# Kernel optimization log

Hardware: AMD Instinct MI355X
Metric: run time of the kernel (lower is better)

The kernel has to match this reference:

```python
import jax, jax.numpy as jnp
import numpy as np

K = 16
NS = [2048, 512, 128]

def _knn(q, r, k):
    # q: [B,M,3] query centers, r: [B,N,3] reference points -> (idx [B,M,k], sqdist [B,M,k])
    d2 = (jnp.sum(q * q, -1)[:, :, None] + jnp.sum(r * r, -1)[:, None, :]
          - 2.0 * jnp.einsum('bmd,bnd->bmn', q, r))
    neg, idx = jax.lax.top_k(-d2, k)
    return idx, jnp.maximum(-neg, 0.0)

def _gather(feat, idx):
    # feat [B,N,C], idx [B,M,k] -> [B,M,k,C]
    return jax.vmap(lambda f, i: f[i])(feat, idx)

def _down(x, pos, n, W1, b1, W2, b2):
    # PointNet++-style TransitionDown: sample n centers, kNN group, rel-pos concat, shared MLP, max-pool
    centers = pos[:, :n]
    idx, _ = _knn(centers, pos, K)
    rel = _gather(pos, idx) - centers[:, :, None, :]           # [B,n,K,3]
    feat = jnp.concatenate([rel, _gather(x, idx)], -1)          # [B,n,K,C+3]
    h = jax.nn.relu(feat @ W1 + b1) @ W2 + b2                   # last_act=False
    return jnp.max(h, axis=2), centers

def _up(xc, pc, prv_feat, prv_pos, W, b):
    # TransitionUp: 3-NN inverse-distance interpolation + skip concat + pointwise conv1d
    idx, d2 = _knn(prv_pos, pc, 3)
    w = 1.0 / (d2 + 1e-8)
    w = w / jnp.sum(w, -1, keepdims=True)
    interp = jnp.sum(_gather(xc, idx) * w[..., None], axis=2)   # [B,Nprv,Cc]
    cat = jnp.concatenate([interp, prv_feat], -1)
    return jax.nn.relu(cat @ W + b)

def setup_inputs() -> dict:
    key = jax.random.key(0)
    ks = jax.random.split(key, 16)
    p = lambda k, s: jax.random.normal(k, s, jnp.float32) * 0.02
    B, N = 4, 8192
    return {
        'x': jax.random.normal(ks[0], (B, N, 3), jnp.float32),
        'pos': jax.random.uniform(ks[1], (B, N, 3), jnp.float32),
        'd0_W1': p(ks[2], (6, 128)),   'd0_b1': jnp.zeros((128,), jnp.float32),
        'd0_W2': p(ks[3], (128, 128)), 'd0_b2': jnp.zeros((128,), jnp.float32),
        'd1_W1': p(ks[4], (131, 256)), 'd1_b1': jnp.zeros((256,), jnp.float32),
        'd1_W2': p(ks[5], (256, 256)), 'd1_b2': jnp.zeros((256,), jnp.float32),
        'd2_W1': p(ks[6], (259, 512)), 'd2_b1': jnp.zeros((512,), jnp.float32),
        'd2_W2': p(ks[7], (512, 512)), 'd2_b2': jnp.zeros((512,), jnp.float32),
        'u0_W': p(ks[8], (768, 256)),  'u0_b': jnp.zeros((256,), jnp.float32),
        'u1_W': p(ks[9], (384, 128)),  'u1_b': jnp.zeros((128,), jnp.float32),
        'u2_W': p(ks[10], (134, 128)), 'u2_b': jnp.zeros((128,), jnp.float32),
        'f_W1': p(ks[11], (128, 128)), 'f_b1': jnp.zeros((128,), jnp.float32),
        'f_W2': p(ks[12], (128, 128)), 'f_b2': jnp.zeros((128,), jnp.float32),
    }

def reference(x, pos, d0_W1, d0_b1, d0_W2, d0_b2, d1_W1, d1_b1, d1_W2, d1_b2,
              d2_W1, d2_b1, d2_W2, d2_b2, u0_W, u0_b, u1_W, u1_b, u2_W, u2_b,
              f_W1, f_b1, f_W2, f_b2):
    pos0, x0 = pos, x
    # encoder (transition-down) with cached (pos, x) per scale
    x1, pos1 = _down(x0, pos0, NS[0], d0_W1, d0_b1, d0_W2, d0_b2)
    x2, pos2 = _down(x1, pos1, NS[1], d1_W1, d1_b1, d1_W2, d1_b2)
    x3, pos3 = _down(x2, pos2, NS[2], d2_W1, d2_b1, d2_W2, d2_b2)
    # decoder (transition-up) consuming the cache in reverse; last level concats raw pos to skip feat
    up = _up(x3, pos3, x2, pos2, u0_W, u0_b)
    up = _up(up, pos2, x1, pos1, u1_W, u1_b)
    prv0 = jnp.concatenate([x0, pos0], -1)
    up = _up(up, pos1, prv0, pos0, u2_W, u2_b)
    # feat_map_layer_out: two pointwise conv1d layers, last_act=False
    out = jax.nn.relu(up @ f_W1 + f_b1) @ f_W2 + f_b2
    return (out, pos0)
```

## Files before the change

kernel.cpp:

```cpp
#include <hip/hip_runtime.h>

#define NFULL 8192
#define BATCH 4

typedef unsigned long long u64;
typedef unsigned int u32;
typedef __attribute__((ext_vector_type(8))) short bf8_t;
typedef __attribute__((ext_vector_type(4))) float f4_t;

__device__ __forceinline__ u32 fbias(float f) {
  u32 u = __float_as_uint(f);
  return (u & 0x80000000u) ? ~u : (u | 0x80000000u);
}
__device__ __forceinline__ float funbias(u32 b) {
  u32 u = (b & 0x80000000u) ? (b & 0x7fffffffu) : ~b;
  return __uint_as_float(u);
}
__device__ __forceinline__ short f2bf(float f) {
  u32 u = __float_as_uint(f);
  u32 r = u + 0x7FFFu + ((u >> 16) & 1u);
  return (short)(r >> 16);
}

__device__ __forceinline__ void group_insert_g32(u32 m32, u64 ck, int slot16,
                                                 u64& val, u64& tau) {
  if (m32) {
    while (m32) {
      int src = __ffs(m32) - 1;
      m32 &= m32 - 1;
      u64 c = __shfl((unsigned long long)ck, src, 32);
      u64 prev = __shfl_up((unsigned long long)val, 1, 16);
      if (slot16 == 0) prev = 0ull;
      val = (val <= c) ? val : ((prev <= c) ? c : prev);
    }
    tau = __shfl((unsigned long long)val, 15, 16);
  }
}

__device__ __forceinline__ void first_round_sort32(u64 ck, int gl,
                                                   u64& val, u64& tau) {
  u64 v = ck;
#pragma unroll
  for (int size = 2; size <= 32; size <<= 1) {
#pragma unroll
    for (int stride = size >> 1; stride > 0; stride >>= 1) {
      u64 other = __shfl_xor((unsigned long long)v, stride, 32);
      bool ddd = ((gl & size) == 0);
      bool takeMin = (((gl & stride) == 0) == ddd);
      u64 mn = (v <= other) ? v : other;
      u64 mx = (v <= other) ? other : v;
      v = takeMin ? mn : mx;
    }
  }
  val = __shfl((unsigned long long)v, gl & 15, 32);
  tau = __shfl((unsigned long long)val, 15, 16);
}

__device__ __forceinline__ void scan_range_g32(const float4* __restrict__ sb,
    int s, int e, float qx, float qy, float qz, float qq,
    int g32, int gl, int slot16, u64& val, u64& tau) {
  for (int t0 = s; t0 < e; t0 += 32) {
    int j = t0 + gl;
    u64 ck = ~0ull;
    if (j < e) {
      float4 P = sb[j];
      float rr = P.x * P.x + P.y * P.y + P.z * P.z;
      float d2 = qq + rr - 2.0f * (qx * P.x + qy * P.y + qz * P.z);
      ck = ((u64)fbias(d2) << 32) | (u32)__float_as_uint(P.w);
    }
    u64 full = __ballot(ck < tau);
    u32 m32 = (u32)(full >> (g32 * 32));
    group_insert_g32(m32, ck, slot16, val, tau);
  }
}

template<int GR, int R, int NREF>
__device__ __forceinline__ void knn_tail16_g32(
    const float4* __restrict__ sb, const int* __restrict__ cs,
    float qx, float qy, float qz, float qq,
    int ix, int iy, int iz, int x0, int x1, int y0, int y1, int z0, int z1,
    int g32, int gl, int slot16, u64& val, u64& tau) {
  const float h = 1.0f / GR;
  float m = 1e30f;
  if (x0 > 0)      m = fminf(m, qx - x0 * h);
  if (x1 < GR - 1) m = fminf(m, (x1 + 1) * h - qx);
  if (y0 > 0)      m = fminf(m, qy - y0 * h);
  if (y1 < GR - 1) m = fminf(m, (y1 + 1) * h - qy);
  if (z0 > 0)      m = fminf(m, qz - z0 * h);
  if (z1 < GR - 1) m = fminf(m, (z1 + 1) * h - qz);
  float bound = m * m;
  float kth_d2 = funbias((u32)(tau >> 32));
  if (!(kth_d2 < bound)) {
    int X0 = max(ix - (R + 1), 0), X1 = min(ix + (R + 1), GR - 1);
    int Y0 = max(iy - (R + 1), 0), Y1 = min(iy + (R + 1), GR - 1);
    int Z0 = max(iz - (R + 1), 0), Z1 = min(iz + (R + 1), GR - 1);
    int NY2 = Y1 - Y0 + 1;
    int nrow2 = (Z1 - Z0 + 1) * NY2;
    for (int rr2 = 0; rr2 < nrow2; ++rr2) {
      int zz = Z0 + rr2 / NY2, yy = Y0 + rr2 % NY2;
      int c0 = (zz * GR + yy) * GR;
      bool mid = (zz >= z0 && zz <= z1 && yy >= y0 && yy <= y1);
      int s1 = cs[c0 + X0];
      int e1 = mid ? cs[c0 + x0] : cs[c0 + X1 + 1];
      scan_range_g32(sb, s1, e1, qx, qy, qz, qq, g32, gl, slot16, val, tau);
      if (mid) {
        int s2 = cs[c0 + x1 + 1];
        int e2 = cs[c0 + X1 + 1];
        scan_range_g32(sb, s2, e2, qx, qy, qz, qq, g32, gl, slot16, val, tau);
      }
    }
    x0 = X0; x1 = X1; y0 = Y0; y1 = Y1; z0 = Z0; z1 = Z1;
    m = 1e30f;
    if (x0 > 0)      m = fminf(m, qx - x0 * h);
    if (x1 < GR - 1) m = fminf(m, (x1 + 1) * h - qx);
    if (y0 > 0)      m = fminf(m, qy - y0 * h);
    if (y1 < GR - 1) m = fminf(m, (y1 + 1) * h - qy);
    if (z0 > 0)      m = fminf(m, qz - z0 * h);
    if (z1 < GR - 1) m = fminf(m, (z1 + 1) * h - qz);
    bound = m * m;
    kth_d2 = funbias((u32)(tau >> 32));
    if (!(kth_d2 < bound)) {
      for (int t0 = 0; t0 < NREF; t0 += 32) {
        int j = t0 + gl;
        u64 ck = ~0ull;
        if (j < NREF) {
          float4 P = sb[j];
          int cx = min(max((int)(P.x * GR), 0), GR - 1);
          int cy = min(max((int)(P.y * GR), 0), GR - 1);
          int cz = min(max((int)(P.z * GR), 0), GR - 1);
          bool inbox = (cx >= x0 && cx <= x1 && cy >= y0 && cy <= y1 &&
                        cz >= z0 && cz <= z1);
          if (!inbox) {
            float rr = P.x * P.x + P.y * P.y + P.z * P.z;
            float d2 = qq + rr - 2.0f * (qx * P.x + qy * P.y + qz * P.z);
            ck = ((u64)fbias(d2) << 32) | (u32)__float_as_uint(P.w);
          }
        }
        u64 full = __ballot(ck < tau);
        u32 m32 = (u32)(full >> (g32 * 32));
        group_insert_g32(m32, ck, slot16, val, tau);
      }
    }
  }
}

template<int GR, int R, int NREF>
__device__ void knn_grid16_g32_dev(int vbx, int b,
    const float* __restrict__ pos, const float4* __restrict__ sorted,
    const int* __restrict__ cellStart, int csStride, int Mq,
    int* __restrict__ oidx) {
  int wv = threadIdx.x >> 6, lane = threadIdx.x & 63;
  int g32 = lane >> 5, gl = lane & 31;
  int q = vbx * 8 + wv * 2 + g32;
  const float* pb = pos + (size_t)b * NFULL * 3;
  const float4* sb = sorted + (size_t)b * NREF;
  const int* cs = cellStart + b * csStride;
  float qx = pb[q * 3 + 0], qy = pb[q * 3 + 1], qz = pb[q * 3 + 2];
  float qq = qx * qx + qy * qy + qz * qz;
  int ix = min(max((int)(qx * GR), 0), GR - 1);
  int iy = min(max((int)(qy * GR), 0), GR - 1);
  int iz = min(max((int)(qz * GR), 0), GR - 1);
  int x0 = max(ix - R, 0), x1 = min(ix + R, GR - 1);
  int y0 = max(iy - R, 0), y1 = min(iy + R, GR - 1);
  int z0 = max(iz - R, 0), z1 = min(iz + R, GR - 1);

  int ny = y1 - y0 + 1;
  int nrow = (z1 - z0 + 1) * ny;
  int s_i = 0, len_i = 0;
  if (gl < nrow) {
    int zz = z0 + gl / ny, yy = y0 + gl % ny;
    int c0 = (zz * GR + yy) * GR + x0;
    s_i = cs[c0];
    len_i = cs[c0 + (x1 - x0) + 1] - s_i;
  }
  int p_i = len_i;
#pragma unroll
  for (int st = 1; st < 32; st <<= 1) {
    int o = __shfl_up(p_i, st, 32);
    if (gl >= st) p_i += o;
  }
  int T = __shfl(p_i, 31, 32);
  p_i -= len_i;
  int d_i = s_i - p_i;
  if (gl >= nrow) p_i = 0x7fffffff;

  int slot16 = lane & 15;
  u64 val, tau;

  {
    int v = gl;
    int r = 0;
#pragma unroll
    for (int st = 16; st >= 1; st >>= 1) {
      int pc = __shfl(p_i, r + st, 32);
      if (v >= pc) r += st;
    }
    int addr = v + __shfl(d_i, r, 32);
    u64 ck = ~0ull;
    if (v < T) {
      float4 P = sb[addr];
      float rr = P.x * P.x + P.y * P.y + P.z * P.z;
      float d2 = qq + rr - 2.0f * (qx * P.x + qy * P.y + qz * P.z);
      ck = ((u64)fbias(d2) << 32) | (u32)__float_as_uint(P.w);
    }
    first_round_sort32(ck, gl, val, tau);
  }

  for (int v0 = 32; v0 < T; v0 += 32) {
    int v = v0 + gl;
    int r = 0;
#pragma unroll
    for (int st = 16; st >= 1; st >>= 1) {
      int pc = __shfl(p_i, r + st, 32);
      if (v >= pc) r += st;
    }
    int addr = v + __shfl(d_i, r, 32);
    u64 ck = ~0ull;
    if (v < T) {
      float4 P = sb[addr];
      float rr = P.x * P.x + P.y * P.y + P.z * P.z;
      float d2 = qq + rr - 2.0f * (qx * P.x + qy * P.y + qz * P.z);
      ck = ((u64)fbias(d2) << 32) | (u32)__float_as_uint(P.w);
    }
    u64 full = __ballot(ck < tau);
    u32 m32 = (u32)(full >> (g32 * 32));
    group_insert_g32(m32, ck, slot16, val, tau);
  }

  knn_tail16_g32<GR, R, NREF>(sb, cs, qx, qy, qz, qq,
      ix, iy, iz, x0, x1, y0, y1, z0, z1, g32, gl, slot16, val, tau);

  if (gl < 16) {
    size_t base = ((size_t)b * Mq + q) * 16;
    oidx[base + gl] = (int)(u32)val;
  }
}

__device__ void knn_brute16_g32_dev(int vbx, int b,
    const float* __restrict__ pos, int Nref, int Mq, int* __restrict__ oidx) {
  int wv = threadIdx.x >> 6, lane = threadIdx.x & 63;
  int g32 = lane >> 5, gl = lane & 31;
  int q = vbx * 8 + wv * 2 + g32;
  const float* pb = pos + (size_t)b * NFULL * 3;
  float qx = pb[q * 3 + 0], qy = pb[q * 3 + 1], qz = pb[q * 3 + 2];
  float qq = qx * qx + qy * qy + qz * qz;

  int slot16 = lane & 15;
  u64 val, tau;

  {
    int j = gl;
    float rx = pb[j * 3 + 0];
    float ry = pb[j * 3 + 1];
    float rz = pb[j * 3 + 2];
    float rr = rx * rx + ry * ry + rz * rz;
    float d2 = qq + rr - 2.0f * (qx * rx + qy * ry + qz * rz);
    u64 ck = ((u64)fbias(d2) << 32) | (u32)j;
    first_round_sort32(ck, gl, val, tau);
  }

  for (int t0 = 32; t0 < Nref; t0 += 32) {
    int j = t0 + gl;
    float rx = pb[j * 3 + 0];
    float ry = pb[j * 3 + 1];
    float rz = pb[j * 3 + 2];
    float rr = rx * rx + ry * ry + rz * rz;
    float d2 = qq + rr - 2.0f * (qx * rx + qy * ry + qz * rz);
    u64 ck = ((u64)fbias(d2) << 32) | (u32)j;
    u64 full = __ballot(ck < tau);
    u32 m32 = (u32)(full >> (g32 * 32));
    group_insert_g32(m32, ck, slot16, val, tau);
  }

  if (gl < 16) {
    size_t base = ((size_t)b * Mq + q) * 16;
    oidx[base + gl] = (int)(u32)val;
  }
}

__device__ __forceinline__ void lane_insert3(u64 ck, u64& v0, u64& v1, u64& v2) {
  u64 a = (v0 <= ck) ? v0 : ck;
  u64 bb = (v0 <= ck) ? ck : v0;
  v0 = a;
  u64 c = (v1 <= bb) ? v1 : bb;
  u64 d = (v1 <= bb) ? bb : v1;
  v1 = c;
  v2 = (v2 <= d) ? v2 : d;
}

__device__ __forceinline__ void merge3(u64 v0, u64 v1, u64 v2,
                                       u64& o0, u64& o1, u64& o2) {
  u64 h = v0;
  int hc = 0;
  u64 outs[3];
#pragma unroll
  for (int k = 0; k < 3; ++k) {
    u64 m = h;
#pragma unroll
    for (int st = 1; st < 16; st <<= 1) {
      u64 o = __shfl_xor((unsigned long long)m, st, 16);
      m = (m <= o) ? m : o;
    }
    outs[k] = m;
    if (h == m) { ++hc; h = (hc == 1) ? v1 : ((hc == 2) ? v2 : ~0ull); }
  }
  o0 = outs[0]; o1 = outs[1]; o2 = outs[2];
}

__device__ __forceinline__ void scan_range3(const float4* __restrict__ sb,
    int s, int e, float qx, float qy, float qz, float qq,
    int gl, u64& v0, u64& v1, u64& v2) {
  for (int t0 = s; t0 < e; t0 += 16) {
    int j = t0 + gl;
    if (j < e) {
      float4 P = sb[j];
      float rr = P.x * P.x + P.y * P.y + P.z * P.z;
      float d2 = qq + rr - 2.0f * (qx * P.x + qy * P.y + qz * P.z);
      u64 ck = ((u64)fbias(d2) << 32) | (u32)__float_as_uint(P.w);
      lane_insert3(ck, v0, v1, v2);
    }
  }
}

template<int GR, int R, int NREF>
__device__ __forceinline__ void knn_tail3(
    const float4* __restrict__ sb, const int* __restrict__ cs,
    float qx, float qy, float qz, float qq,
    int ix, int iy, int iz, int x0, int x1, int y0, int y1, int z0, int z1,
    int gl, u64& v0, u64& v1, u64& v2, u64& o0, u64& o1, u64& o2) {
  const float h = 1.0f / GR;
  float m = 1e30f;
  if (x0 > 0)      m = fminf(m, qx - x0 * h);
  if (x1 < GR - 1) m = fminf(m, (x1 + 1) * h - qx);
  if (y0 > 0)      m = fminf(m, qy - y0 * h);
  if (y1 < GR - 1) m = fminf(m, (y1 + 1) * h - qy);
  if (z0 > 0)      m = fminf(m, qz - z0 * h);
  if (z1 < GR - 1) m = fminf(m, (z1 + 1) * h - qz);
  float bound = m * m;
  merge3(v0, v1, v2, o0, o1, o2);
  float kth_d2 = funbias((u32)(o2 >> 32));
  if (!(kth_d2 < bound)) {
    int X0 = max(ix - (R + 1), 0), X1 = min(ix + (R + 1), GR - 1);
    int Y0 = max(iy - (R + 1), 0), Y1 = min(iy + (R + 1), GR - 1);
    int Z0 = max(iz - (R + 1), 0), Z1 = min(iz + (R + 1), GR - 1);
    int NY2 = Y1 - Y0 + 1;
    int nrow2 = (Z1 - Z0 + 1) * NY2;
    for (int rr2 = 0; rr2 < nrow2; ++rr2) {
      int zz = Z0 + rr2 / NY2, yy = Y0 + rr2 % NY2;
      int c0 = (zz * GR + yy) * GR;
      bool mid = (zz >= z0 && zz <= z1 && yy >= y0 && yy <= y1);
      int s1 = cs[c0 + X0];
      int e1 = mid ? cs[c0 + x0] : cs[c0 + X1 + 1];
      scan_range3(sb, s1, e1, qx, qy, qz, qq, gl, v0, v1, v2);
      if (mid) {
        int s2 = cs[c0 + x1 + 1];
        int e2 = cs[c0 + X1 + 1];
        scan_range3(sb, s2, e2, qx, qy, qz, qq, gl, v0, v1, v2);
      }
    }
    x0 = X0; x1 = X1; y0 = Y0; y1 = Y1; z0 = Z0; z1 = Z1;
    m = 1e30f;
    if (x0 > 0)      m = fminf(m, qx - x0 * h);
    if (x1 < GR - 1) m = fminf(m, (x1 + 1) * h - qx);
    if (y0 > 0)      m = fminf(m, qy - y0 * h);
    if (y1 < GR - 1) m = fminf(m, (y1 + 1) * h - qy);
    if (z0 > 0)      m = fminf(m, qz - z0 * h);
    if (z1 < GR - 1) m = fminf(m, (z1 + 1) * h - qz);
    bound = m * m;
    merge3(v0, v1, v2, o0, o1, o2);
    kth_d2 = funbias((u32)(o2 >> 32));
    if (!(kth_d2 < bound)) {
      for (int t0 = 0; t0 < NREF; t0 += 16) {
        int j = t0 + gl;
        if (j < NREF) {
          float4 P = sb[j];
          int cx = min(max((int)(P.x * GR), 0), GR - 1);
          int cy = min(max((int)(P.y * GR), 0), GR - 1);
          int cz = min(max((int)(P.z * GR), 0), GR - 1);
          bool inbox = (cx >= x0 && cx <= x1 && cy >= y0 && cy <= y1 &&
                        cz >= z0 && cz <= z1);
          if (!inbox) {
            float rr = P.x * P.x + P.y * P.y + P.z * P.z;
            float d2 = qq + rr - 2.0f * (qx * P.x + qy * P.y + qz * P.z);
            u64 ck = ((u64)fbias(d2) << 32) | (u32)__float_as_uint(P.w);
            lane_insert3(ck, v0, v1, v2);
          }
        }
// ... 174 lines not shown
  float qx = pb[q * 3 + 0], qy = pb[q * 3 + 1], qz = pb[q * 3 + 2];
  float qq = qx * qx + qy * qy + qz * qz;

  u64 v0 = ~0ull, v1 = ~0ull, v2 = ~0ull;
  for (int j = gl; j < Nref; j += 16) {
    float rx = pb[j * 3 + 0];
    float ry = pb[j * 3 + 1];
    float rz = pb[j * 3 + 2];
    float rr = rx * rx + ry * ry + rz * rz;
    float d2 = qq + rr - 2.0f * (qx * rx + qy * ry + qz * rz);
    u64 ck = ((u64)fbias(d2) << 32) | (u32)j;
    lane_insert3(ck, v0, v1, v2);
  }
  u64 o0, o1, o2;
  merge3(v0, v1, v2, o0, o1, o2);

  if (gl < 3) {
    u64 val = (gl == 0) ? o0 : ((gl == 1) ? o1 : o2);
    size_t base = ((size_t)b * Mq + q) * 3;
    oidx[base + gl] = (int)(u32)val;
    od2[base + gl] = fmaxf(funbias((u32)(val >> 32)), 0.0f);
  }
}

__device__ __forceinline__ void pack_tile_rt(const float* __restrict__ W,
                                             short* __restrict__ outp,
                                             int KDIM, int N, int tile, int lane) {
  int NT = N >> 4;
  int kt = tile / NT, nt = tile - kt * NT;
  int n = nt * 16 + (lane & 15);
  int k0 = kt * 32 + (lane >> 4) * 8;
  bf8_t v;
#pragma unroll
  for (int j = 0; j < 8; ++j) {
    int k = k0 + j;
    v[j] = (k < KDIM) ? f2bf(W[(size_t)k * N + n]) : (short)0;
  }
  *(bf8_t*)(outp + ((size_t)tile * 64 + lane) * 8) = v;
}

__device__ void pack_dispatch(int blk, int lane,
    const float* d0W1, short* d0W1p, const float* d0W2, short* d0W2p,
    const float* d1W1, short* d1W1p, const float* d1W2, short* d1W2p,
    const float* d2W1, short* d2W1p, const float* d2W2, short* d2W2p,
    const float* u2W, short* u2Wp, const float* fW1, short* fW1p,
    const float* fW2, short* fW2p,
    const float* u0W, short* u0Wp, const float* u1W, short* u1Wp,
    const float* pos, float* posOut) {
  if      (blk < 8)    pack_tile_rt(d0W1, d0W1p, 6, 128, blk, lane);
  else if (blk < 40)   pack_tile_rt(d0W2, d0W2p, 128, 128, blk - 8, lane);
  else if (blk < 120)  pack_tile_rt(d1W1, d1W1p, 131, 256, blk - 40, lane);
  else if (blk < 248)  pack_tile_rt(d1W2, d1W2p, 256, 256, blk - 120, lane);
  else if (blk < 536)  pack_tile_rt(d2W1, d2W1p, 259, 512, blk - 248, lane);
  else if (blk < 1048) pack_tile_rt(d2W2, d2W2p, 512, 512, blk - 536, lane);
  else if (blk < 1088) pack_tile_rt(u2W, u2Wp, 134, 128, blk - 1048, lane);
  else if (blk < 1120) pack_tile_rt(fW1, fW1p, 128, 128, blk - 1088, lane);
  else if (blk < 1152) pack_tile_rt(fW2, fW2p, 128, 128, blk - 1120, lane);
  else if (blk < 1536) pack_tile_rt(u0W, u0Wp, 768, 256, blk - 1152, lane);
  else if (blk < 1632) pack_tile_rt(u1W, u1Wp, 384, 128, blk - 1536, lane);
  else {
    int base = (blk - 1632) * 256;
#pragma unroll
    for (int j = 0; j < 4; ++j) {
      int i = base + lane + j * 64;
      posOut[i] = pos[i];
    }
  }
}

__global__ __launch_bounds__(256) void pre_kernel(
    const float* __restrict__ pos, float4* __restrict__ sortedA,
    int* __restrict__ csA, float4* __restrict__ sortedB, int* __restrict__ csB,
    float4* __restrict__ sortedC, int* __restrict__ csC,
    const float* d0W1, short* d0W1p, const float* d0W2, short* d0W2p,
    const float* d1W1, short* d1W1p, const float* d1W2, short* d1W2p,
    const float* d2W1, short* d2W1p, const float* d2W2, short* d2W2p,
    const float* u2W, short* u2Wp, const float* fW1, short* fW1p,
    const float* fW2, short* fW2p,
    const float* u0W, short* u0Wp, const float* u1W, short* u1Wp,
    float* posOut,
    int* __restrict__ idx2, int* __restrict__ idxu0, float* __restrict__ d2u0) {
  __shared__ int cnt[4096];
  __shared__ int partial[256];
  int bx = blockIdx.x, t = threadIdx.x;
  if (bx >= 580) {
    int i = bx - 580;
    knn_brute3_dev(i & 31, i >> 5, pos, 128, 512, idxu0, d2u0);
    return;
  }
  if (bx >= 516) {
    int i = bx - 516;
    knn_brute16_g32_dev(i & 15, i >> 4, pos, 512, 128, idx2);
    return;
  }
  if (bx >= 12) {
    int tt = (bx - 12) * 4 + (t >> 6);
    pack_dispatch(tt, t & 63,
        d0W1, d0W1p, d0W2, d0W2p, d1W1, d1W1p, d1W2, d1W2p,
        d2W1, d2W1p, d2W2, d2W2p, u2W, u2Wp, fW1, fW1p, fW2, fW2p,
        u0W, u0Wp, u1W, u1Wp, pos, posOut);
    return;
  }
  int which = bx >> 2, b = bx & 3;
  int NREF = (which == 0) ? 8192 : (which == 1) ? 2048 : 512;
  int GR = (which == 0) ? 16 : 8;
  int NC = GR * GR * GR;
  float4* sorted = ((which == 0) ? sortedA : (which == 1) ? sortedB : sortedC)
                   + (size_t)b * NREF;
  int* cs = ((which == 0) ? csA + b * 4097 : (which == 1) ? csB + b * 513
                                           : csC + b * 513);
  const float* pb = pos + (size_t)b * NFULL * 3;
  for (int c = t; c < NC; c += 256) cnt[c] = 0;
  __syncthreads();
  for (int p = t; p < NREF; p += 256) {
    float x = pb[p * 3 + 0], y = pb[p * 3 + 1], z = pb[p * 3 + 2];
    int cx = min(max((int)(x * GR), 0), GR - 1);
    int cy = min(max((int)(y * GR), 0), GR - 1);
    int cz = min(max((int)(z * GR), 0), GR - 1);
    atomicAdd(&cnt[(cz * GR + cy) * GR + cx], 1);
  }
  __syncthreads();
  int chunk = (NC + 255) / 256;
  int s = 0;
  for (int i = 0; i < chunk; ++i) {
    int c = t * chunk + i;
    if (c < NC) s += cnt[c];
  }
  partial[t] = s;
  __syncthreads();
  if (t == 0) {
    int run = 0;
    for (int i = 0; i < 256; ++i) { int v = partial[i]; partial[i] = run; run += v; }
  }
  __syncthreads();
  int run = partial[t];
  for (int i = 0; i < chunk; ++i) {
    int c = t * chunk + i;
    if (c < NC) { int v = cnt[c]; cnt[c] = run; run += v; }
  }
  __syncthreads();
  for (int c = t; c < NC; c += 256) cs[c] = cnt[c];
  if (t == 0) cs[NC] = NREF;
  __syncthreads();
  for (int p = t; p < NREF; p += 256) {
    float x = pb[p * 3 + 0], y = pb[p * 3 + 1], z = pb[p * 3 + 2];
    int cx = min(max((int)(x * GR), 0), GR - 1);
    int cy = min(max((int)(y * GR), 0), GR - 1);
    int cz = min(max((int)(z * GR), 0), GR - 1);
    int slot = atomicAdd(&cnt[(cz * GR + cy) * GR + cx], 1);
    sorted[slot] = make_float4(x, y, z, __uint_as_float((u32)p));
  }
}

__global__ __launch_bounds__(256) void knn16_kernel(
    const float* __restrict__ pos,
    const float4* __restrict__ sortedA, const int* __restrict__ csA,
    const float4* __restrict__ sortedB, const int* __restrict__ csB,
    int* __restrict__ idx0, int* __restrict__ idx1) {
  int bx = blockIdx.x, b = blockIdx.y;
  if (bx < 64)
    knn_grid16_g32_dev<8, 2, 2048>(bx, b, pos, sortedB, csB, 513, 512, idx1);
  else
    knn_grid16_g32_dev<16, 2, 8192>(bx - 64, b, pos, sortedA, csA, 4097, 2048, idx0);
}

template<int FEAT, int CIN, int CHID, int FPAD, int QB, int WAVES>
__device__ void down_mfma_body(int bxx, int b,
    const float* __restrict__ pos, const float* __restrict__ xin,
    const int* __restrict__ idx,
    const short* __restrict__ W1p, const float* __restrict__ b1,
    const short* __restrict__ W2p, const float* __restrict__ b2,
    float* __restrict__ out, int n, int nprev) {
  const int KT1 = FPAD / 32, NT1 = CHID / 16;
  const int KT2 = CHID / 32, NT2 = CHID / 16;
  __shared__ short sFeat[QB][16][FPAD + 8];
  __shared__ short sH1[QB][16][CHID + 8];
  __shared__ int sIdx[QB][16];
  __shared__ float sCtr[QB][3];
  int q0 = bxx * QB;
  int t = threadIdx.x;
  int lane = t & 63, wv = t >> 6;
  const float* pb = pos + (size_t)b * NFULL * 3;
  const float* xb = xin + (size_t)b * nprev * CIN;
  if (t < QB * 16)
    sIdx[t >> 4][t & 15] = idx[((size_t)b * n + q0 + (t >> 4)) * 16 + (t & 15)];
  if (t < QB * 3) sCtr[t / 3][t % 3] = pb[(q0 + t / 3) * 3 + (t % 3)];
  __syncthreads();
  for (int e = t; e < QB * 16 * FPAD; e += 64 * WAVES) {
    int k = e / FPAD, c = e - k * FPAD;
    int qq = k >> 4, kk = k & 15;
    float v = 0.f;
    if (c < 3) v = pb[sIdx[qq][kk] * 3 + c] - sCtr[qq][c];
    else if (c < FEAT) v = xb[(size_t)sIdx[qq][kk] * CIN + (c - 3)];
    sFeat[qq][kk][c] = f2bf(v);
  }
  __syncthreads();

  int col = lane & 15, quad = lane >> 4;
  const bf8_t* W1t = (const bf8_t*)W1p;
  for (int nt = 2 * wv; nt < NT1; nt += 2 * WAVES) {
    f4_t acc[QB][2];
    float bb0 = b1[nt * 16 + col], bb1 = b1[nt * 16 + 16 + col];
#pragma unroll
    for (int q = 0; q < QB; ++q) {
      acc[q][0] = {bb0, bb0, bb0, bb0};
      acc[q][1] = {bb1, bb1, bb1, bb1};
    }
#pragma unroll
    for (int kt = 0; kt < KT1; ++kt) {
      bf8_t bf0 = W1t[(kt * NT1 + nt) * 64 + lane];
      bf8_t bf1 = W1t[(kt * NT1 + nt + 1) * 64 + lane];
#pragma unroll
      for (int q = 0; q < QB; ++q) {
        bf8_t a = *(const bf8_t*)&sFeat[q][col][kt * 32 + quad * 8];
        acc[q][0] = __builtin_amdgcn_mfma_f32_16x16x32_bf16(a, bf0, acc[q][0], 0, 0, 0);
        acc[q][1] = __builtin_amdgcn_mfma_f32_16x16x32_bf16(a, bf1, acc[q][1], 0, 0, 0);
      }
    }
#pragma unroll
    for (int q = 0; q < QB; ++q)
#pragma unroll
      for (int r = 0; r < 4; ++r) {
        sH1[q][quad * 4 + r][nt * 16 + col] = f2bf(fmaxf(acc[q][0][r], 0.f));
        sH1[q][quad * 4 + r][nt * 16 + 16 + col] = f2bf(fmaxf(acc[q][1][r], 0.f));
      }
  }
  __syncthreads();

  const bf8_t* W2t = (const bf8_t*)W2p;
  for (int nt = 2 * wv; nt < NT2; nt += 2 * WAVES) {
    f4_t acc[QB][2];
    float bb0 = b2[nt * 16 + col], bb1 = b2[nt * 16 + 16 + col];
#pragma unroll
    for (int q = 0; q < QB; ++q) {
      acc[q][0] = {bb0, bb0, bb0, bb0};
      acc[q][1] = {bb1, bb1, bb1, bb1};
    }
#pragma unroll
    for (int kt = 0; kt < KT2; ++kt) {
      bf8_t bf0 = W2t[(kt * NT2 + nt) * 64 + lane];
      bf8_t bf1 = W2t[(kt * NT2 + nt + 1) * 64 + lane];
#pragma unroll
      for (int q = 0; q < QB; ++q) {
        bf8_t a = *(const bf8_t*)&sH1[q][col][kt * 32 + quad * 8];
        acc[q][0] = __builtin_amdgcn_mfma_f32_16x16x32_bf16(a, bf0, acc[q][0], 0, 0, 0);
        acc[q][1] = __builtin_amdgcn_mfma_f32_16x16x32_bf16(a, bf1, acc[q][1], 0, 0, 0);
      }
    }
#pragma unroll
    for (int q = 0; q < QB; ++q) {
      float m0 = fmaxf(fmaxf(acc[q][0][0], acc[q][0][1]), fmaxf(acc[q][0][2], acc[q][0][3]));
      float m1 = fmaxf(fmaxf(acc[q][1][0], acc[q][1][1]), fmaxf(acc[q][1][2], acc[q][1][3]));
      m0 = fmaxf(m0, __shfl_xor(m0, 16, 64));
      m0 = fmaxf(m0, __shfl_xor(m0, 32, 64));
      m1 = fmaxf(m1, __shfl_xor(m1, 16, 64));
      m1 = fmaxf(m1, __shfl_xor(m1, 32, 64));
      if (lane < 16) {
        float* ob = out + ((size_t)b * n + q0 + q) * CHID;
        ob[nt * 16 + lane] = m0;
        ob[nt * 16 + 16 + lane] = m1;
      }
    }
  }
}

template<int FEAT, int CIN, int CHID, int FPAD, int QB, int WAVES>
__global__ __launch_bounds__(64 * WAVES) void down_mfma_kernel(
    const float* __restrict__ pos, const float* __restrict__ xin,
    const int* __restrict__ idx,
    const short* __restrict__ W1p, const float* __restrict__ b1,
    const short* __restrict__ W2p, const float* __restrict__ b2,
    float* __restrict__ out, int n, int nprev) {
  down_mfma_body<FEAT, CIN, CHID, FPAD, QB, WAVES>(blockIdx.x, blockIdx.y,
      pos, xin, idx, W1p, b1, W2p, b2, out, n, nprev);
}

__global__ __launch_bounds__(256) void down0_knn3_kernel(
    const float* __restrict__ pos, const float* __restrict__ xin,
    const int* __restrict__ idx,
    const short* __restrict__ W1p, const float* __restrict__ b1,
    const short* __restrict__ W2p, const float* __restrict__ b2,
    float* __restrict__ out,
    const float4* __restrict__ sortedB, const int* __restrict__ csB,
    const float4* __restrict__ sortedC, const int* __restrict__ csC,
    int* __restrict__ idxu1, float* __restrict__ d2u1,
    int* __restrict__ idxu2, float* __restrict__ d2u2) {
  int bx = blockIdx.x, b = blockIdx.y;
  if (bx < 512)
    down_mfma_body<6, 3, 128, 32, 4, 4>(bx, b, pos, xin, idx,
        W1p, b1, W2p, b2, out, 2048, 8192);
  else if (bx < 1024)
    knn_grid_flat3_dev<8, 1, 2048>(bx - 512, b, pos, sortedB, csB, 513, 8192, idxu2, d2u2);
  else
    knn_grid_flat32_3_dev<8, 2, 512>(bx - 1024, b, pos, sortedC, csC, 513, 2048, idxu1, d2u1);
}

template<int CIN, int CPRV, int COUT, int WPB>
__global__ __launch_bounds__(64 * WPB) void up_mfma_kernel(
    const float* __restrict__ xc, int ncoarse,
    const int* __restrict__ idx3, const float* __restrict__ d23,
    const float* __restrict__ prv, const short* __restrict__ Wp,
    const float* __restrict__ bvec, float* __restrict__ out, int m) {
  const int CTOT = CIN + CPRV;
  const int KT = CTOT / 32, NT = COUT / 16;
  __shared__ short sA[16][CTOT + 8];
  __shared__ float sWt[16][3];
  __shared__ int   sIt[16][3];
  int b = blockIdx.y, q0 = blockIdx.x * 16, t = threadIdx.x;
  int lane = t & 63, wv = t >> 6;
  if (t < 16) {
    size_t base = ((size_t)b * m + q0 + t) * 3;
    float d0 = d23[base + 0], d1 = d23[base + 1], d2v = d23[base + 2];
    float w0 = 1.f / (d0 + 1e-8f), w1 = 1.f / (d1 + 1e-8f), w2 = 1.f / (d2v + 1e-8f);
    float s = w0 + w1 + w2;
    sWt[t][0] = w0 / s; sWt[t][1] = w1 / s; sWt[t][2] = w2 / s;
    sIt[t][0] = idx3[base + 0]; sIt[t][1] = idx3[base + 1]; sIt[t][2] = idx3[base + 2];
  }
  __syncthreads();
  const float* xb = xc + (size_t)b * ncoarse * CIN;
  const float* pvb = prv + ((size_t)b * m + q0) * CPRV;
  for (int e = t; e < 16 * CIN; e += 64 * WPB) {
    int p = e / CIN, c = e % CIN;
    float v = sWt[p][0] * xb[(size_t)sIt[p][0] * CIN + c]
            + sWt[p][1] * xb[(size_t)sIt[p][1] * CIN + c]
            + sWt[p][2] * xb[(size_t)sIt[p][2] * CIN + c];
    sA[p][c] = f2bf(v);
  }
  for (int e = t; e < 16 * CPRV; e += 64 * WPB) {
    int p = e / CPRV, c = e % CPRV;
    sA[p][CIN + c] = f2bf(pvb[(size_t)p * CPRV + c]);
  }
  __syncthreads();
  int col = lane & 15, quad = lane >> 4;
  const bf8_t* Wt = (const bf8_t*)Wp;
  float* ob = out + ((size_t)b * m + q0) * COUT;
  for (int nt = 2 * wv; nt < NT; nt += 2 * WPB) {
    float bb0 = bvec[nt * 16 + col], bb1 = bvec[nt * 16 + 16 + col];
    f4_t acc0 = {bb0, bb0, bb0, bb0}, acc1 = {bb1, bb1, bb1, bb1};
#pragma unroll
    for (int kt = 0; kt < KT; ++kt) {
      bf8_t a = *(const bf8_t*)&sA[col][kt * 32 + quad * 8];
      bf8_t bf0 = Wt[(kt * NT + nt) * 64 + lane];
      bf8_t bf1 = Wt[(kt * NT + nt + 1) * 64 + lane];
      acc0 = __builtin_amdgcn_mfma_f32_16x16x32_bf16(a, bf0, acc0, 0, 0, 0);
      acc1 = __builtin_amdgcn_mfma_f32_16x16x32_bf16(a, bf1, acc1, 0, 0, 0);
    }
#pragma unroll
    for (int r = 0; r < 4; ++r) {
      ob[(size_t)(quad * 4 + r) * COUT + nt * 16 + col] = fmaxf(acc0[r], 0.f);
      ob[(size_t)(quad * 4 + r) * COUT + nt * 16 + 16 + col] = fmaxf(acc1[r], 0.f);
    }
  }
}

__global__ __launch_bounds__(128) void up2f_mfma_kernel(
    const float* __restrict__ xc,
    const int* __restrict__ idx3, const float* __restrict__ d23,
    const float* __restrict__ x0, const float* __restrict__ pos0,
    const short* __restrict__ u2Wp, const float* __restrict__ u2b,
    const short* __restrict__ fW1p, const float* __restrict__ fb1,
    const short* __restrict__ fW2p, const float* __restrict__ fb2,
    float* __restrict__ out) {
  __shared__ short sA[16][168];
  __shared__ short sB[16][136];
  __shared__ float sWt[16][3];
  __shared__ int   sIt[16][3];
  int b = blockIdx.y, q0 = blockIdx.x * 16, t = threadIdx.x;
  int lane = t & 63, wv = t >> 6;
  if (t < 16) {
    size_t base = ((size_t)b * NFULL + q0 + t) * 3;
    float d0 = d23[base + 0], d1 = d23[base + 1], d2v = d23[base + 2];
    float w0 = 1.f / (d0 + 1e-8f), w1 = 1.f / (d1 + 1e-8f), w2 = 1.f / (d2v + 1e-8f);
    float s = w0 + w1 + w2;
    sWt[t][0] = w0 / s; sWt[t][1] = w1 / s; sWt[t][2] = w2 / s;
    sIt[t][0] = idx3[base + 0]; sIt[t][1] = idx3[base + 1]; sIt[t][2] = idx3[base + 2];
  }
  __syncthreads();
  const float* xb = xc + (size_t)b * 2048 * 128;
#pragma unroll
  for (int p = 0; p < 16; ++p) {
    float v = sWt[p][0] * xb[(size_t)sIt[p][0] * 128 + t]
            + sWt[p][1] * xb[(size_t)sIt[p][1] * 128 + t]
            + sWt[p][2] * xb[(size_t)sIt[p][2] * 128 + t];
    sA[p][t] = f2bf(v);
  }
  for (int e = t; e < 16 * 32; e += 128) {
    int p = e / 32, c = 128 + (e % 32);
    float v = 0.f;
    if (c < 131) v = x0[((size_t)b * NFULL + q0 + p) * 3 + (c - 128)];
    else if (c < 134) v = pos0[((size_t)b * NFULL + q0 + p) * 3 + (c - 131)];
    sA[p][c] = f2bf(v);
  }
  __syncthreads();
  int col = lane & 15, quad = lane >> 4;

  bf8_t a1[5];
#pragma unroll
  for (int kt = 0; kt < 5; ++kt)
    a1[kt] = *(const bf8_t*)&sA[col][kt * 32 + quad * 8];
  const bf8_t* W1t = (const bf8_t*)u2Wp;
  for (int nt = 2 * wv; nt < 8; nt += 4) {
    float bb0 = u2b[nt * 16 + col], bb1 = u2b[nt * 16 + 16 + col];
    f4_t acc0 = {bb0, bb0, bb0, bb0}, acc1 = {bb1, bb1, bb1, bb1};
#pragma unroll
    for (int kt = 0; kt < 5; ++kt) {
      bf8_t bf0 = W1t[(kt * 8 + nt) * 64 + lane];
      bf8_t bf1 = W1t[(kt * 8 + nt + 1) * 64 + lane];
      acc0 = __builtin_amdgcn_mfma_f32_16x16x32_bf16(a1[kt], bf0, acc0, 0, 0, 0);
      acc1 = __builtin_amdgcn_mfma_f32_16x16x32_bf16(a1[kt], bf1, acc1, 0, 0, 0);
    }
#pragma unroll
    for (int r = 0; r < 4; ++r) {
      sB[quad * 4 + r][nt * 16 + col] = f2bf(fmaxf(acc0[r], 0.f));
      sB[quad * 4 + r][nt * 16 + 16 + col] = f2bf(fmaxf(acc1[r], 0.f));
    }
  }
  __syncthreads();

  bf8_t a2[4];
#pragma unroll
  for (int kt = 0; kt < 4; ++kt)
    a2[kt] = *(const bf8_t*)&sB[col][kt * 32 + quad * 8];
  const bf8_t* W2t = (const bf8_t*)fW1p;
  for (int nt = 2 * wv; nt < 8; nt += 4) {
    float bb0 = fb1[nt * 16 + col], bb1 = fb1[nt * 16 + 16 + col];
    f4_t acc0 = {bb0, bb0, bb0, bb0}, acc1 = {bb1, bb1, bb1, bb1};
#pragma unroll
    for (int kt = 0; kt < 4; ++kt) {
      bf8_t bf0 = W2t[(kt * 8 + nt) * 64 + lane];
      bf8_t bf1 = W2t[(kt * 8 + nt + 1) * 64 + lane];
      acc0 = __builtin_amdgcn_mfma_f32_16x16x32_bf16(a2[kt], bf0, acc0, 0, 0, 0);
      acc1 = __builtin_amdgcn_mfma_f32_16x16x32_bf16(a2[kt], bf1, acc1, 0, 0, 0);
    }
#pragma unroll
    for (int r = 0; r < 4; ++r) {
      sA[quad * 4 + r][nt * 16 + col] = f2bf(fmaxf(acc0[r], 0.f));
      sA[quad * 4 + r][nt * 16 + 16 + col] = f2bf(fmaxf(acc1[r], 0.f));
    }
  }
  __syncthreads();

  bf8_t a3[4];
#pragma unroll
  for (int kt = 0; kt < 4; ++kt)
    a3[kt] = *(const bf8_t*)&sA[col][kt * 32 + quad * 8];
  const bf8_t* W3t = (const bf8_t*)fW2p;
  float* ob = out + ((size_t)b * NFULL + q0) * 128;
  for (int nt = 2 * wv; nt < 8; nt += 4) {
    float bb0 = fb2[nt * 16 + col], bb1 = fb2[nt * 16 + 16 + col];
    f4_t acc0 = {bb0, bb0, bb0, bb0}, acc1 = {bb1, bb1, bb1, bb1};
#pragma unroll
    for (int kt = 0; kt < 4; ++kt) {
      bf8_t bf0 = W3t[(kt * 8 + nt) * 64 + lane];
      bf8_t bf1 = W3t[(kt * 8 + nt + 1) * 64 + lane];
      acc0 = __builtin_amdgcn_mfma_f32_16x16x32_bf16(a3[kt], bf0, acc0, 0, 0, 0);
      acc1 = __builtin_amdgcn_mfma_f32_16x16x32_bf16(a3[kt], bf1, acc1, 0, 0, 0);
    }
#pragma unroll
    for (int r = 0; r < 4; ++r) {
      ob[(size_t)(quad * 4 + r) * 128 + nt * 16 + col] = acc0[r];
      ob[(size_t)(quad * 4 + r) * 128 + nt * 16 + 16 + col] = acc1[r];
    }
  }
}

extern "C" void kernel_launch(void* const* d_in, const int* in_sizes, int n_in,
                              void* d_out, int out_size, void* d_ws, size_t ws_size,
                              hipStream_t stream) {
  const float* x    = (const float*)d_in[0];
  const float* pos  = (const float*)d_in[1];
  const float* d0W1 = (const float*)d_in[2];
  const float* d0b1 = (const float*)d_in[3];
  const float* d0W2 = (const float*)d_in[4];
  const float* d0b2 = (const float*)d_in[5];
  const float* d1W1 = (const float*)d_in[6];
  const float* d1b1 = (const float*)d_in[7];
  const float* d1W2 = (const float*)d_in[8];
  const float* d1b2 = (const float*)d_in[9];
  const float* d2W1 = (const float*)d_in[10];
  const float* d2b1 = (const float*)d_in[11];
  const float* d2W2 = (const float*)d_in[12];
  const float* d2b2 = (const float*)d_in[13];
  const float* u0W  = (const float*)d_in[14];
  const float* u0b  = (const float*)d_in[15];
  const float* u1W  = (const float*)d_in[16];
  const float* u1b  = (const float*)d_in[17];
  const float* u2W  = (const float*)d_in[18];
  const float* u2b  = (const float*)d_in[19];
  const float* fW1  = (const float*)d_in[20];
  const float* fb1  = (const float*)d_in[21];
  const float* fW2  = (const float*)d_in[22];
  const float* fb2  = (const float*)d_in[23];

  char* ws = (char*)d_ws;
  float* x1    = (float*)(ws + 0);
  float* x2    = (float*)(ws + 4194304);
  float* x3    = (float*)(ws + 6291456);
  float* up0o  = (float*)(ws + 7340032);
  float* up1o  = (float*)(ws + 9437184);
  int*   idx0  = (int*)  (ws + 13631488);
  int*   idx1  = (int*)  (ws + 14155776);
  int*   idx2  = (int*)  (ws + 14286848);
  float4* sortedC = (float4*)(ws + 14319616);
  int*    csC     = (int*)   (ws + 14352384);
  int*   idxu0 = (int*)  (ws + 14843904);
  float* d2u0  = (float*)(ws + 14868480);
  int*   idxu1 = (int*)  (ws + 14893056);
  float* d2u1  = (float*)(ws + 14991360);
  int*   idxu2 = (int*)  (ws + 15089664);
  float* d2u2  = (float*)(ws + 15482880);
  short* d1W1p = (short*)(ws + 15876096);
  short* d1W2p = (short*)(ws + 15958016);
  short* d2W1p = (short*)(ws + 16089088);
  short* d2W2p = (short*)(ws + 16384000);
  short* d0W1p = (short*)(ws + 16908288);
  short* d0W2p = (short*)(ws + 16916480);
  float4* sortedA = (float4*)(ws + 16949248);
  int*    csA     = (int*)   (ws + 17473536);
  float4* sortedB = (float4*)(ws + 17539136);
  int*    csB     = (int*)   (ws + 17670208);
  short* u2Wp  = (short*)(ws + 17697920);
  short* fW1p  = (short*)(ws + 17738880);
  short* fW2p  = (short*)(ws + 17771648);

  float* out = (float*)d_out;
  short* u0Wp = (short*)out;
  short* u1Wp = (short*)(out + 98304);

  pre_kernel<<<dim3(708), 256, 0, stream>>>(
      pos, sortedA, csA, sortedB, csB, sortedC, csC,
      d0W1, d0W1p, d0W2, d0W2p, d1W1, d1W1p, d1W2, d1W2p,
      d2W1, d2W1p, d2W2, d2W2p, u2W, u2Wp, fW1, fW1p, fW2, fW2p,
      u0W, u0Wp, u1W, u1Wp,
      out + (size_t)BATCH * NFULL * 128,
      idx2, idxu0, d2u0);

  knn16_kernel<<<dim3(320, BATCH), 256, 0, stream>>>(
      pos, sortedA, csA, sortedB, csB, idx0, idx1);

  down0_knn3_kernel<<<dim3(1152, BATCH), 256, 0, stream>>>(
      pos, x, idx0, d0W1p, d0b1, d0W2p, d0b2, x1,
      sortedB, csB, sortedC, csC, idxu1, d2u1, idxu2, d2u2);

  down_mfma_kernel<131, 128, 256, 160, 4, 8><<<dim3(128, BATCH), 512, 0, stream>>>(
      pos, x1, idx1, d1W1p, d1b1, d1W2p, d1b2, x2, 512, 2048);
  down_mfma_kernel<259, 256, 512, 288, 2, 8><<<dim3(64, BATCH), 512, 0, stream>>>(
      pos, x2, idx2, d2W1p, d2b1, d2W2p, d2b2, x3, 128, 512);

  up_mfma_kernel<512, 256, 256, 4><<<dim3(32, BATCH), 256, 0, stream>>>(
      x3, 128, idxu0, d2u0, x2, u0Wp, u0b, up0o, 512);
  up_mfma_kernel<256, 128, 128, 2><<<dim3(128, BATCH), 128, 0, stream>>>(
      up0o, 512, idxu1, d2u1, x1, u1Wp, u1b, up1o, 2048);
  up2f_mfma_kernel<<<dim3(512, BATCH), 128, 0, stream>>>(
      up1o, idxu2, d2u2, x, pos, u2Wp, u2b, fW1p, fb1, fW2p, fb2, out);
}
```

Baseline: 293.5 us.

## Use full-wave kNN16 search and move 3-NN searches into kNN kernel

The k=16 grid kNN now gives each query a whole 64-lane wavefront instead of a 32-lane half-wave. That halves the number of candidate-chunk iterations and uses a 64-wide bitonic first round, at the cost of twice as many blocks and half the queries per wave. The 3-NN upsampling searches move out of the fused down0 kernel and into the kNN kernel, so down0 now runs as a standalone MFMA kernel. This rebalances work between the two launches but changes how the wavefront-serial insertion loop scales with candidate density.

```diff
diff --git a/kernel.cpp b/kernel.cpp
--- a/kernel.cpp
+++ b/kernel.cpp
@@ -37,6 +37,21 @@
   }
 }
 
+__device__ __forceinline__ void group_insert_g64(u64 m64, u64 ck, int slot16,
+                                                 u64& val, u64& tau) {
+  if (m64) {
+    while (m64) {
+      int src = __ffsll((unsigned long long)m64) - 1;
+      m64 &= m64 - 1;
+      u64 c = __shfl((unsigned long long)ck, src, 64);
+      u64 prev = __shfl_up((unsigned long long)val, 1, 16);
+      if (slot16 == 0) prev = 0ull;
+      val = (val <= c) ? val : ((prev <= c) ? c : prev);
+    }
+    tau = __shfl((unsigned long long)val, 15, 16);
+  }
+}
+
 __device__ __forceinline__ void first_round_sort32(u64 ck, int gl,
                                                    u64& val, u64& tau) {
   u64 v = ck;
@@ -56,11 +71,30 @@
   tau = __shfl((unsigned long long)val, 15, 16);
 }
 
-__device__ __forceinline__ void scan_range_g32(const float4* __restrict__ sb,
+__device__ __forceinline__ void first_round_sort64(u64 ck, int gl,
+                                                   u64& val, u64& tau) {
+  u64 v = ck;
+#pragma unroll
+  for (int size = 2; size <= 64; size <<= 1) {
+#pragma unroll
+    for (int stride = size >> 1; stride > 0; stride >>= 1) {
+      u64 other = __shfl_xor((unsigned long long)v, stride, 64);
+      bool ddd = ((gl & size) == 0);
+      bool takeMin = (((gl & stride) == 0) == ddd);
+      u64 mn = (v <= other) ? v : other;
+      u64 mx = (v <= other) ? other : v;
+      v = takeMin ? mn : mx;
+    }
+  }
+  val = __shfl((unsigned long long)v, gl & 15, 64);
+  tau = __shfl((unsigned long long)val, 15, 16);
+}
+
+__device__ __forceinline__ void scan_range_g64(const float4* __restrict__ sb,
     int s, int e, float qx, float qy, float qz, float qq,
-    int g32, int gl, int slot16, u64& val, u64& tau) {
-  for (int t0 = s; t0 < e; t0 += 32) {
-    int j = t0 + gl;
+    int lane, int slot16, u64& val, u64& tau) {
+  for (int t0 = s; t0 < e; t0 += 64) {
+    int j = t0 + lane;
     u64 ck = ~0ull;
     if (j < e) {
       float4 P = sb[j];
@@ -68,18 +102,17 @@
       float d2 = qq + rr - 2.0f * (qx * P.x + qy * P.y + qz * P.z);
       ck = ((u64)fbias(d2) << 32) | (u32)__float_as_uint(P.w);
     }
-    u64 full = __ballot(ck < tau);
-    u32 m32 = (u32)(full >> (g32 * 32));
-    group_insert_g32(m32, ck, slot16, val, tau);
+    u64 m64 = __ballot(ck < tau);
+    group_insert_g64(m64, ck, slot16, val, tau);
   }
 }
 
 template<int GR, int R, int NREF>
-__device__ __forceinline__ void knn_tail16_g32(
+__device__ __forceinline__ void knn_tail16_g64(
     const float4* __restrict__ sb, const int* __restrict__ cs,
     float qx, float qy, float qz, float qq,
     int ix, int iy, int iz, int x0, int x1, int y0, int y1, int z0, int z1,
-    int g32, int gl, int slot16, u64& val, u64& tau) {
+    int lane, int slot16, u64& val, u64& tau) {
   const float h = 1.0f / GR;
   float m = 1e30f;
   if (x0 > 0)      m = fminf(m, qx - x0 * h);
@@ -102,11 +135,11 @@
       bool mid = (zz >= z0 && zz <= z1 && yy >= y0 && yy <= y1);
       int s1 = cs[c0 + X0];
       int e1 = mid ? cs[c0 + x0] : cs[c0 + X1 + 1];
-      scan_range_g32(sb, s1, e1, qx, qy, qz, qq, g32, gl, slot16, val, tau);
+      scan_range_g64(sb, s1, e1, qx, qy, qz, qq, lane, slot16, val, tau);
       if (mid) {
         int s2 = cs[c0 + x1 + 1];
         int e2 = cs[c0 + X1 + 1];
-        scan_range_g32(sb, s2, e2, qx, qy, qz, qq, g32, gl, slot16, val, tau);
+        scan_range_g64(sb, s2, e2, qx, qy, qz, qq, lane, slot16, val, tau);
       }
     }
     x0 = X0; x1 = X1; y0 = Y0; y1 = Y1; z0 = Z0; z1 = Z1;
@@ -120,8 +153,8 @@
     bound = m * m;
     kth_d2 = funbias((u32)(tau >> 32));
     if (!(kth_d2 < bound)) {
-      for (int t0 = 0; t0 < NREF; t0 += 32) {
-        int j = t0 + gl;
+      for (int t0 = 0; t0 < NREF; t0 += 64) {
+        int j = t0 + lane;
         u64 ck = ~0ull;
         if (j < NREF) {
           float4 P = sb[j];
@@ -136,22 +169,20 @@
             ck = ((u64)fbias(d2) << 32) | (u32)__float_as_uint(P.w);
           }
         }
-        u64 full = __ballot(ck < tau);
-        u32 m32 = (u32)(full >> (g32 * 32));
-        group_insert_g32(m32, ck, slot16, val, tau);
+        u64 m64 = __ballot(ck < tau);
+        group_insert_g64(m64, ck, slot16, val, tau);
       }
     }
   }
 }
 
 template<int GR, int R, int NREF>
-__device__ void knn_grid16_g32_dev(int vbx, int b,
+__device__ void knn_grid16_g64_dev(int vbx, int b,
     const float* __restrict__ pos, const float4* __restrict__ sorted,
     const int* __restrict__ cellStart, int csStride, int Mq,
     int* __restrict__ oidx) {
   int wv = threadIdx.x >> 6, lane = threadIdx.x & 63;
-  int g32 = lane >> 5, gl = lane & 31;
-  int q = vbx * 8 + wv * 2 + g32;
+  int q = vbx * 4 + wv;
   const float* pb = pos + (size_t)b * NFULL * 3;
   const float4* sb = sorted + (size_t)b * NREF;
   const int* cs = cellStart + b * csStride;
@@ -167,35 +198,35 @@
   int ny = y1 - y0 + 1;
   int nrow = (z1 - z0 + 1) * ny;
   int s_i = 0, len_i = 0;
-  if (gl < nrow) {
-    int zz = z0 + gl / ny, yy = y0 + gl % ny;
+  if (lane < nrow) {
+    int zz = z0 + lane / ny, yy = y0 + lane % ny;
     int c0 = (zz * GR + yy) * GR + x0;
     s_i = cs[c0];
     len_i = cs[c0 + (x1 - x0) + 1] - s_i;
   }
   int p_i = len_i;
 #pragma unroll
-  for (int st = 1; st < 32; st <<= 1) {
-    int o = __shfl_up(p_i, st, 32);
-    if (gl >= st) p_i += o;
-  }
-  int T = __shfl(p_i, 31, 32);
+  for (int st = 1; st < 64; st <<= 1) {
+    int o = __shfl_up(p_i, st, 64);
+    if (lane >= st) p_i += o;
+  }
+  int T = __shfl(p_i, 63, 64);
   p_i -= len_i;
   int d_i = s_i - p_i;
-  if (gl >= nrow) p_i = 0x7fffffff;
+  if (lane >= nrow) p_i = 0x7fffffff;
 
   int slot16 = lane & 15;
   u64 val, tau;
 
   {
-    int v = gl;
+    int v = lane;
     int r = 0;
 #pragma unroll
-    for (int st = 16; st >= 1; st >>= 1) {
-      int pc = __shfl(p_i, r + st, 32);
+    for (int st = 32; st >= 1; st >>= 1) {
+      int pc = __shfl(p_i, r + st, 64);
       if (v >= pc) r += st;
     }
-    int addr = v + __shfl(d_i, r, 32);
+    int addr = v + __shfl(d_i, r, 64);
     u64 ck = ~0ull;
     if (v < T) {
       float4 P = sb[addr];
@@ -203,18 +234,18 @@
       float d2 = qq + rr - 2.0f * (qx * P.x + qy * P.y + qz * P.z);
       ck = ((u64)fbias(d2) << 32) | (u32)__float_as_uint(P.w);
     }
-    first_round_sort32(ck, gl, val, tau);
-  }
-
-  for (int v0 = 32; v0 < T; v0 += 32) {
-    int v = v0 + gl;
+    first_round_sort64(ck, lane, val, tau);
+  }
+
+  for (int v0 = 64; v0 < T; v0 += 64) {
+    int v = v0 + lane;
     int r = 0;
 #pragma unroll
-    for (int st = 16; st >= 1; st >>= 1) {
-      int pc = __shfl(p_i, r + st, 32);
+    for (int st = 32; st >= 1; st >>= 1) {
+      int pc = __shfl(p_i, r + st, 64);
       if (v >= pc) r += st;
     }
-    int addr = v + __shfl(d_i, r, 32);
+    int addr = v + __shfl(d_i, r, 64);
     u64 ck = ~0ull;
     if (v < T) {
       float4 P = sb[addr];
@@ -222,17 +253,16 @@
       float d2 = qq + rr - 2.0f * (qx * P.x + qy * P.y + qz * P.z);
       ck = ((u64)fbias(d2) << 32) | (u32)__float_as_uint(P.w);
     }
-    u64 full = __ballot(ck < tau);
-    u32 m32 = (u32)(full >> (g32 * 32));
-    group_insert_g32(m32, ck, slot16, val, tau);
-  }
-
-  knn_tail16_g32<GR, R, NREF>(sb, cs, qx, qy, qz, qq,
-      ix, iy, iz, x0, x1, y0, y1, z0, z1, g32, gl, slot16, val, tau);
-
-  if (gl < 16) {
+    u64 m64 = __ballot(ck < tau);
+    group_insert_g64(m64, ck, slot16, val, tau);
+  }
+
+  knn_tail16_g64<GR, R, NREF>(sb, cs, qx, qy, qz, qq,
+      ix, iy, iz, x0, x1, y0, y1, z0, z1, lane, slot16, val, tau);
+
+  if (lane < 16) {
     size_t base = ((size_t)b * Mq + q) * 16;
-    oidx[base + gl] = (int)(u32)val;
+    oidx[base + lane] = (int)(u32)val;
   }
 }
 
@@ -713,20 +743,27 @@
   }
 }
 
-__global__ __launch_bounds__(256) void knn16_kernel(
+__global__ __launch_bounds__(256) void knn_kernel(
     const float* __restrict__ pos,
     const float4* __restrict__ sortedA, const int* __restrict__ csA,
     const float4* __restrict__ sortedB, const int* __restrict__ csB,
-    int* __restrict__ idx0, int* __restrict__ idx1) {
+    const float4* __restrict__ sortedC, const int* __restrict__ csC,
+    int* __restrict__ idx0, int* __restrict__ idx1,
+    int* __restrict__ idxu1, float* __restrict__ d2u1,
+    int* __restrict__ idxu2, float* __restrict__ d2u2) {
   int bx = blockIdx.x, b = blockIdx.y;
-  if (bx < 64)
-    knn_grid16_g32_dev<8, 2, 2048>(bx, b, pos, sortedB, csB, 513, 512, idx1);
+  if (bx < 128)
+    knn_grid16_g64_dev<8, 2, 2048>(bx, b, pos, sortedB, csB, 513, 512, idx1);
+  else if (bx < 640)
+    knn_grid16_g64_dev<16, 2, 8192>(bx - 128, b, pos, sortedA, csA, 4097, 2048, idx0);
+  else if (bx < 768)
+    knn_grid_flat32_3_dev<8, 2, 512>(bx - 640, b, pos, sortedC, csC, 513, 2048, idxu1, d2u1);
   else
-    knn_grid16_g32_dev<16, 2, 8192>(bx - 64, b, pos, sortedA, csA, 4097, 2048, idx0);
+    knn_grid_flat3_dev<8, 1, 2048>(bx - 768, b, pos, sortedB, csB, 513, 8192, idxu2, d2u2);
 }
 
 template<int FEAT, int CIN, int CHID, int FPAD, int QB, int WAVES>
-__device__ void down_mfma_body(int bxx, int b,
+__global__ __launch_bounds__(64 * WAVES) void down_mfma_kernel(
     const float* __restrict__ pos, const float* __restrict__ xin,
     const int* __restrict__ idx,
     const short* __restrict__ W1p, const float* __restrict__ b1,
@@ -738,7 +775,7 @@
   __shared__ short sH1[QB][16][CHID + 8];
   __shared__ int sIdx[QB][16];
   __shared__ float sCtr[QB][3];
-  int q0 = bxx * QB;
+  int b = blockIdx.y, q0 = blockIdx.x * QB;
   int t = threadIdx.x;
   int lane = t & 63, wv = t >> 6;
   const float* pb = pos + (size_t)b * NFULL * 3;
@@ -823,37 +860,6 @@
       }
     }
   }
-}
-
-template<int FEAT, int CIN, int CHID, int FPAD, int QB, int WAVES>
-__global__ __launch_bounds__(64 * WAVES) void down_mfma_kernel(
-    const float* __restrict__ pos, const float* __restrict__ xin,
-    const int* __restrict__ idx,
-    const short* __restrict__ W1p, const float* __restrict__ b1,
-    const short* __restrict__ W2p, const float* __restrict__ b2,
-    float* __restrict__ out, int n, int nprev) {
-  down_mfma_body<FEAT, CIN, CHID, FPAD, QB, WAVES>(blockIdx.x, blockIdx.y,
-      pos, xin, idx, W1p, b1, W2p, b2, out, n, nprev);
-}
-
-__global__ __launch_bounds__(256) void down0_knn3_kernel(
-    const float* __restrict__ pos, const float* __restrict__ xin,
-    const int* __restrict__ idx,
-    const short* __restrict__ W1p, const float* __restrict__ b1,
-    const short* __restrict__ W2p, const float* __restrict__ b2,
-    float* __restrict__ out,
-    const float4* __restrict__ sortedB, const int* __restrict__ csB,
-    const float4* __restrict__ sortedC, const int* __restrict__ csC,
-    int* __restrict__ idxu1, float* __restrict__ d2u1,
-    int* __restrict__ idxu2, float* __restrict__ d2u2) {
-  int bx = blockIdx.x, b = blockIdx.y;
-  if (bx < 512)
-    down_mfma_body<6, 3, 128, 32, 4, 4>(bx, b, pos, xin, idx,
-        W1p, b1, W2p, b2, out, 2048, 8192);
-  else if (bx < 1024)
-    knn_grid_flat3_dev<8, 1, 2048>(bx - 512, b, pos, sortedB, csB, 513, 8192, idxu2, d2u2);
-  else
-    knn_grid_flat32_3_dev<8, 2, 512>(bx - 1024, b, pos, sortedC, csC, 513, 2048, idxu1, d2u1);
 }
 
 template<int CIN, int CPRV, int COUT, int WPB>
@@ -1096,13 +1102,12 @@
       out + (size_t)BATCH * NFULL * 128,
       idx2, idxu0, d2u0);
 
-  knn16_kernel<<<dim3(320, BATCH), 256, 0, stream>>>(
-      pos, sortedA, csA, sortedB, csB, idx0, idx1);
-
-  down0_knn3_kernel<<<dim3(1152, BATCH), 256, 0, stream>>>(
-      pos, x, idx0, d0W1p, d0b1, d0W2p, d0b2, x1,
-      sortedB, csB, sortedC, csC, idxu1, d2u1, idxu2, d2u2);
-
+  knn_kernel<<<dim3(1280, BATCH), 256, 0, stream>>>(
+      pos, sortedA, csA, sortedB, csB, sortedC, csC,
+      idx0, idx1, idxu1, d2u1, idxu2, d2u2);
+
+  down_mfma_kernel<6, 3, 128, 32, 4, 4><<<dim3(512, BATCH), 256, 0, stream>>>(
+      pos, x, idx0, d0W1p, d0b1, d0W2p, d0b2, x1, 2048, 8192);
   down_mfma_kernel<131, 128, 256, 160, 4, 8><<<dim3(128, BATCH), 512, 0, stream>>>(
       pos, x1, idx1, d1W1p, d1b1, d1W2p, d1b2, x2, 512, 2048);
   down_mfma_kernel<259, 256, 512, 288, 2, 8><<<dim3(64, BATCH), 512, 0, stream>>>(
```

Result: no change. 289.7 us (-1.3%).
